# Performance work log

Hardware: AMD Instinct MI355X
Metric: run time of the kernel (lower is better)

## Reference

```python
import jax, jax.numpy as jnp
import numpy as np

NUM_HEADS = 8
HEAD_DIM = 64
EMBED = NUM_HEADS * HEAD_DIM  # 512
KERNEL = 4
TOP_K = 8
SCALING = HEAD_DIM ** (-0.5)


def setup_inputs() -> dict:
    key = jax.random.key(0)
    ks = jax.random.split(key, 5)
    b, s = 4, 4096
    hidden_states = jax.random.normal(ks[0], (b, s, EMBED), dtype=jnp.float32)
    init = 1.0 / np.sqrt(EMBED)
    Wq = jax.random.normal(ks[1], (EMBED, EMBED), dtype=jnp.float32) * init
    Wk = jax.random.normal(ks[2], (EMBED, EMBED), dtype=jnp.float32) * init
    Wv = jax.random.normal(ks[3], (EMBED, EMBED), dtype=jnp.float32) * init
    Wo = jax.random.normal(ks[4], (EMBED, EMBED), dtype=jnp.float32) * init
    return {"hidden_states": hidden_states, "Wq": Wq, "Wk": Wk, "Wv": Wv, "Wo": Wo}


def reference(hidden_states, Wq, Wk, Wv, Wo):
    b, s, _ = hidden_states.shape
    # Q/K/V projections, split heads: (b, s, h, d)
    q = (hidden_states @ Wq).reshape(b, s, NUM_HEADS, HEAD_DIM)
    k = (hidden_states @ Wk).reshape(b, s, NUM_HEADS, HEAD_DIM)
    v = (hidden_states @ Wv).reshape(b, s, NUM_HEADS, HEAD_DIM)

    # KVCachePooling: chunk-mean along seq (s divisible by KERNEL, no pad)
    nc = s // KERNEL
    pooled_k = k.reshape(b, nc, KERNEL, NUM_HEADS, HEAD_DIM).mean(axis=2)  # (b, nc, h, d)
    pooled_v = v.reshape(b, nc, KERNEL, NUM_HEADS, HEAD_DIM).mean(axis=2)

    # TopKSparseRouter: routing scores (b, h, s, nc), reduce heads(max) then queries(max)
    qh = jnp.transpose(q, (0, 2, 1, 3))  # (b, h, s, d)
    route = jnp.einsum('bhsd,bchd->bhsc', qh, pooled_k) * SCALING
    route = route.max(axis=1).max(axis=1)  # (b, nc)
    _, top_idx = jax.lax.top_k(route, TOP_K)  # (b, k)

    # Gather selected pooled chunks: (b, k, h, d)
    k_sel = jnp.take_along_axis(pooled_k, top_idx[:, :, None, None], axis=1)
    v_sel = jnp.take_along_axis(pooled_v, top_idx[:, :, None, None], axis=1)

    # Sparse attention over the k selected chunks only
    attn = jnp.einsum('bhsd,bkhd->bhsk', qh, k_sel) * SCALING  # (b, h, s, k)
    attn = jax.nn.softmax(attn, axis=-1)
    out = jnp.einsum('bhsk,bkhd->bhsd', attn, v_sel)  # (b, h, s, d)
    out = jnp.transpose(out, (0, 2, 1, 3)).reshape(b, s, EMBED)
    return out @ Wo
```

## Files before the change

kernel.cpp:

```cpp
#include <hip/hip_runtime.h>

#define SEQ 4096
#define BATCH 4
#define EMB 512
#define NHEAD 8
#define HDIM 64
#define NCHUNK 1024
#define TOPK 8
#define NSEL 32
#define SCALING 0.125f

typedef unsigned int uint;
typedef unsigned short ushort_t;
typedef __attribute__((ext_vector_type(8))) short short8;
typedef __attribute__((ext_vector_type(4))) float f32x4;
typedef __attribute__((ext_vector_type(4))) unsigned short us4;
typedef __attribute__((ext_vector_type(8))) unsigned short us8;

__device__ __forceinline__ ushort_t bf16_rn(float x) {
  uint b = __float_as_uint(x);
  return (ushort_t)((b + 0x7FFFu + ((b >> 16) & 1u)) >> 16);
}
__device__ __forceinline__ float bf16_f(ushort_t u) {
  return __uint_as_float(((uint)u) << 16);
}

__device__ __forceinline__ void load_lds16(const void* g, void* l) {
  __builtin_amdgcn_global_load_lds(
      (const __attribute__((address_space(1))) unsigned int*)g,
      (__attribute__((address_space(3))) unsigned int*)l, 16, 0, 0);
}

__device__ __forceinline__ f32x4 mfma16(short8 a, short8 b, f32x4 c) {
  return __builtin_amdgcn_mfma_f32_16x16x32_bf16(a, b, c, 0, 0, 0);
}

__device__ __forceinline__ uint float_key(float f) {
  uint bits = __float_as_uint(f);
  return (bits & 0x80000000u) ? ~bits : (bits | 0x80000000u);
}

__global__ __launch_bounds__(256) void wtrans_kernel(
    const float* __restrict__ Wq, const float* __restrict__ Wk,
    const float* __restrict__ Wv,
    ushort_t* __restrict__ Wtq_h, ushort_t* __restrict__ Wtq_l,
    ushort_t* __restrict__ Wtkv_h, ushort_t* __restrict__ Wtkv_l) {
  __shared__ float t[64][65];
  const int z = blockIdx.z;
  const float* src = (z == 0) ? Wq : (z == 1) ? Wk : Wv;
  ushort_t* dh = (z == 0) ? Wtq_h : Wtkv_h;
  ushort_t* dl = (z == 0) ? Wtq_l : Wtkv_l;
  const size_t obase = (z == 2) ? (size_t)512 * 512 : 0;
  const int k0 = blockIdx.x * 64, n0 = blockIdx.y * 64;
  const int tid = threadIdx.x;
#pragma unroll
  for (int i = 0; i < 4; ++i) {
    int row = (tid >> 4) + i * 16, col = (tid & 15) * 4;
    float4 v = *(const float4*)&src[(size_t)(k0 + row) * 512 + n0 + col];
    t[row][col + 0] = v.x; t[row][col + 1] = v.y;
    t[row][col + 2] = v.z; t[row][col + 3] = v.w;
  }
  __syncthreads();
#pragma unroll
  for (int i = 0; i < 4; ++i) {
    int nrow = (tid >> 4) + i * 16, kcol = (tid & 15) * 4;
    us4 h, l;
#pragma unroll
    for (int j = 0; j < 4; ++j) {
      float v = t[kcol + j][nrow];
      ushort_t hb = bf16_rn(v);
      h[j] = hb;
      l[j] = bf16_rn(v - bf16_f(hb));
    }
    size_t o = obase + (size_t)(n0 + nrow) * 512 + k0 + kcol;
    *(us4*)&dh[o] = h;
    *(us4*)&dl[o] = l;
  }
}

__global__ __launch_bounds__(256) void pool_split_kernel(
    const float* __restrict__ H, ushort_t* __restrict__ Hh,
    ushort_t* __restrict__ Hl, ushort_t* __restrict__ Hph,
    ushort_t* __restrict__ Hpl, uint* __restrict__ route) {
  const int idx = blockIdx.x * 256 + threadIdx.x;
  if (idx < BATCH * NCHUNK) route[idx] = 0;
  const int e4 = (idx & 127) << 2;
  const int c = (idx >> 7) & 1023;
  const int b = idx >> 17;
  const size_t rbase = ((size_t)(b * SEQ + c * 4)) * 512 + e4;
  float4 s = make_float4(0.f, 0.f, 0.f, 0.f);
#pragma unroll
  for (int j = 0; j < 4; ++j) {
    float4 v = *(const float4*)&H[rbase + (size_t)j * 512];
    s.x += v.x; s.y += v.y; s.z += v.z; s.w += v.w;
    us4 h, l;
    float a[4] = {v.x, v.y, v.z, v.w};
#pragma unroll
    for (int q = 0; q < 4; ++q) {
      ushort_t hb = bf16_rn(a[q]);
      h[q] = hb;
      l[q] = bf16_rn(a[q] - bf16_f(hb));
    }
    *(us4*)&Hh[rbase + (size_t)j * 512] = h;
    *(us4*)&Hl[rbase + (size_t)j * 512] = l;
  }
  float a[4] = {s.x * 0.25f, s.y * 0.25f, s.z * 0.25f, s.w * 0.25f};
  us4 h, l;
#pragma unroll
  for (int q = 0; q < 4; ++q) {
    ushort_t hb = bf16_rn(a[q]);
    h[q] = hb;
    l[q] = bf16_rn(a[q] - bf16_f(hb));
  }
  size_t po = ((size_t)(b * NCHUNK + c)) * 512 + e4;
  *(us4*)&Hph[po] = h;
  *(us4*)&Hpl[po] = l;
}

__global__ __launch_bounds__(256) void proj_kernel(
    const ushort_t* __restrict__ Hh, const ushort_t* __restrict__ Hl,
    const ushort_t* __restrict__ Hph, const ushort_t* __restrict__ Hpl,
    const ushort_t* __restrict__ Wtq_h, const ushort_t* __restrict__ Wtq_l,
    const ushort_t* __restrict__ Wtkv_h, const ushort_t* __restrict__ Wtkv_l,
    ushort_t* __restrict__ Qh, ushort_t* __restrict__ Ql,
    ushort_t* __restrict__ Pkvh, ushort_t* __restrict__ Pkvl) {
  __shared__ ushort_t lds[2][4][4096];
  const int bid = blockIdx.x;
  const ushort_t *A0, *A1, *B0, *B1;
  ushort_t *Ch, *Cl;
  int ldc, row0, col0;
  if (bid < 512) {
    row0 = (bid >> 2) * 128; col0 = (bid & 3) * 128;
    A0 = Hh; A1 = Hl; B0 = Wtq_h; B1 = Wtq_l; Ch = Qh; Cl = Ql; ldc = 512;
  } else {
    int b2 = bid - 512;
    row0 = (b2 >> 3) * 128; col0 = (b2 & 7) * 128;
    A0 = Hph; A1 = Hpl; B0 = Wtkv_h; B1 = Wtkv_l; Ch = Pkvh; Cl = Pkvl;
    ldc = 1024;
  }
  A0 += (size_t)row0 * 512; A1 += (size_t)row0 * 512;
  B0 += (size_t)col0 * 512; B1 += (size_t)col0 * 512;
  const int tid = threadIdx.x, lane = tid & 63, wv = tid >> 6;
  const int l15 = lane & 15, g = lane >> 4;
  const int wm = wv >> 1, wn = wv & 1;
  f32x4 acc[4][4];
#pragma unroll
  for (int m = 0; m < 4; ++m)
#pragma unroll
    for (int n = 0; n < 4; ++n) acc[m][n] = (f32x4){0.f, 0.f, 0.f, 0.f};

  auto stage = [&](int buf, int t) {
#pragma unroll
    for (int j = 0; j < 2; ++j) {
      int si = j * 256 + wv * 64 + lane;
      int row = si >> 2;
      int kb = ((si & 3) << 4) ^ (((row >> 1) & 3) << 4);
      size_t goff = (size_t)row * 512 + t * 32 + (kb >> 1);
      int doff = (j * 256 + wv * 64) * 8;
      load_lds16(A0 + goff, &lds[buf][0][doff]);
      load_lds16(B0 + goff, &lds[buf][1][doff]);
      load_lds16(A1 + goff, &lds[buf][2][doff]);
      load_lds16(B1 + goff, &lds[buf][3][doff]);
    }
  };

  stage(0, 0);
  int cur = 0;
  for (int t = 0; t < 16; ++t) {
    __syncthreads();
    if (t < 15) stage(cur ^ 1, t + 1);
    short8 ah[4], bh[4], al[4], bl[4];
#pragma unroll
    for (int m = 0; m < 4; ++m) {
      int r = wm * 64 + m * 16 + l15;
      int kb = (g << 4) ^ (((r >> 1) & 3) << 4);
      ah[m] = *(const short8*)&lds[cur][0][r * 32 + (kb >> 1)];
      al[m] = *(const short8*)&lds[cur][2][r * 32 + (kb >> 1)];
    }
#pragma unroll
    for (int n = 0; n < 4; ++n) {
      int r = wn * 64 + n * 16 + l15;
      int kb = (g << 4) ^ (((r >> 1) & 3) << 4);
      bh[n] = *(const short8*)&lds[cur][1][r * 32 + (kb >> 1)];
      bl[n] = *(const short8*)&lds[cur][3][r * 32 + (kb >> 1)];
    }
#pragma unroll
    for (int m = 0; m < 4; ++m)
#pragma unroll
      for (int n = 0; n < 4; ++n) {
        acc[m][n] = mfma16(ah[m], bh[n], acc[m][n]);
        acc[m][n] = mfma16(ah[m], bl[n], acc[m][n]);
        acc[m][n] = mfma16(al[m], bh[n], acc[m][n]);
      }
    cur ^= 1;
  }
#pragma unroll
  for (int m = 0; m < 4; ++m)
#pragma unroll
    for (int n = 0; n < 4; ++n)
#pragma unroll
      for (int q = 0; q < 4; ++q) {
        int row = row0 + wm * 64 + m * 16 + g * 4 + q;
        int col = col0 + wn * 64 + n * 16 + l15;
        float v = acc[m][n][q];
        size_t o = (size_t)row * ldc + col;
        ushort_t hb = bf16_rn(v);
        Ch[o] = hb;
        Cl[o] = bf16_rn(v - bf16_f(hb));
      }
}

__device__ __forceinline__ void stage128x64(const ushort_t* src, int stride,
                                            ushort_t* dst, int wv, int lane) {
#pragma unroll
  for (int j = 0; j < 4; ++j) {
    int si = j * 256 + wv * 64 + lane;
    int row = si >> 3;
    int kb = ((si & 7) << 4) ^ ((row & 7) << 4);
    load_lds16(src + (size_t)row * stride + (kb >> 1),
               dst + (size_t)(j * 256 + wv * 64) * 8);
  }
}

__global__ __launch_bounds__(256) void route_screen(
    const ushort_t* __restrict__ Qh, const ushort_t* __restrict__ Pkh,
    uint* __restrict__ route) {
  __shared__ ushort_t Alds[2][128 * 64];
  __shared__ ushort_t Blds[128 * 64];
  __shared__ float red[2][128];
  const int tid = threadIdx.x, lane = tid & 63, wv = tid >> 6;
  const int l15 = lane & 15, g = lane >> 4;
  const int wm = wv >> 1, wc = wv & 1;
  const int c0 = blockIdx.x * 128;
  const int h = blockIdx.y >> 1, sb = blockIdx.y & 1;
  const int b = blockIdx.z;
  const int s0 = sb * 2048;
  const ushort_t* Qhb = Qh + ((size_t)b * SEQ) * 512 + h * 64;
  const ushort_t* Pkhb = Pkh + ((size_t)(b * NCHUNK + c0)) * 1024 + h * 64;

  stage128x64(Pkhb, 1024, &Blds[0], wv, lane);
  __syncthreads();
  short8 bh[2][4];
#pragma unroll
  for (int kk = 0; kk < 2; ++kk)
#pragma unroll
    for (int n = 0; n < 4; ++n) {
      int r = wc * 64 + n * 16 + l15;
      int kb = (kk * 64 + (g << 4)) ^ ((r & 7) << 4);
      bh[kk][n] = *(const short8*)&Blds[r * 64 + (kb >> 1)];
    }

  float rmax[4] = {-1e30f, -1e30f, -1e30f, -1e30f};
  stage128x64(Qhb + (size_t)s0 * 512, 512, &Alds[0][0], wv, lane);
  int cur = 0;
  for (int it = 0; it < 16; ++it) {
    __syncthreads();
    if (it < 15) {
      size_t so = (size_t)(s0 + (it + 1) * 128) * 512;
      stage128x64(Qhb + so, 512, &Alds[cur ^ 1][0], wv, lane);
    }
    f32x4 acc[4][4];
#pragma unroll
    for (int m = 0; m < 4; ++m)
#pragma unroll
      for (int n = 0; n < 4; ++n) acc[m][n] = (f32x4){0.f, 0.f, 0.f, 0.f};
#pragma unroll
    for (int kk = 0; kk < 2; ++kk) {
      short8 ah[4];
#pragma unroll
      for (int m = 0; m < 4; ++m) {
        int r = wm * 64 + m * 16 + l15;
        int kb = (kk * 64 + (g << 4)) ^ ((r & 7) << 4);
        ah[m] = *(const short8*)&Alds[cur][r * 64 + (kb >> 1)];
      }
#pragma unroll
      for (int m = 0; m < 4; ++m)
#pragma unroll
        for (int n = 0; n < 4; ++n)
          acc[m][n] = mfma16(ah[m], bh[kk][n], acc[m][n]);
    }
#pragma unroll
    for (int n = 0; n < 4; ++n)
#pragma unroll
      for (int m = 0; m < 4; ++m)
        rmax[n] = fmaxf(rmax[n],
                        fmaxf(fmaxf(acc[m][n][0], acc[m][n][1]),
                              fmaxf(acc[m][n][2], acc[m][n][3])));
    cur ^= 1;
  }
#pragma unroll
  for (int n = 0; n < 4; ++n) {
    float v = rmax[n];
    v = fmaxf(v, __shfl_xor(v, 16, 64));
    v = fmaxf(v, __shfl_xor(v, 32, 64));
    if (g == 0) red[wm][wc * 64 + n * 16 + l15] = v;
  }
  __syncthreads();
  if (tid < 128) {
    float v = fmaxf(red[0][tid], red[1][tid]);
    atomicMax(&route[b * NCHUNK + c0 + tid], float_key(v));
  }
}

__global__ __launch_bounds__(256) void topk_sel(const uint* __restrict__ route,
                                                int* __restrict__ cand,
                                                uint* __restrict__ route2) {
  const int b = blockIdx.x, tid = threadIdx.x;
  __shared__ unsigned long long keys[NCHUNK];
#pragma unroll
  for (int i = 0; i < 4; ++i) {
    int idx = tid + i * 256;
    keys[idx] = ((unsigned long long)route[b * NCHUNK + idx] << 32) |
                (uint)(NCHUNK - 1 - idx);
  }
  if (tid < NSEL) route2[b * NSEL + tid] = 0;
  __syncthreads();
  for (int k = 2; k <= NCHUNK; k <<= 1) {
    for (int j = k >> 1; j > 0; j >>= 1) {
#pragma unroll
      for (int ii = 0; ii < 4; ++ii) {
        int i = tid + ii * 256;
        int p = i ^ j;
        if (p > i) {
          bool desc = ((i & k) == 0);
          unsigned long long a = keys[i], c = keys[p];
          bool sw = desc ? (a < c) : (a > c);
          if (sw) { keys[i] = c; keys[p] = a; }
        }
      }
      __syncthreads();
    }
  }
  if (tid < NSEL)
    cand[b * NSEL + tid] = NCHUNK - 1 - (int)(keys[tid] & 0xffffffffu);
}

__global__ __launch_bounds__(256) void rescore_kernel(
    const ushort_t* __restrict__ Qh, const ushort_t* __restrict__ Ql,
    const ushort_t* __restrict__ Pkvh, const ushort_t* __restrict__ Pkvl,
    const int* __restrict__ cand, uint* __restrict__ route2) {
  __shared__ ushort_t Ah[128 * 64], Al[128 * 64];
  __shared__ ushort_t Bh[NSEL * 64], Bl[NSEL * 64];
  __shared__ float red[4][NSEL];
  const int tid = threadIdx.x, lane = tid & 63, wv = tid >> 6;
  const int l15 = lane & 15, g = lane >> 4;
  const int st = blockIdx.x, h = blockIdx.y, b = blockIdx.z;
  const int s0 = st * 128;
  {
    int row = tid >> 3;
    int kb = ((tid & 7) << 4) ^ ((row & 7) << 4);
    int c = cand[b * NSEL + row];
    size_t src = ((size_t)(b * NCHUNK + c)) * 1024 + h * 64 + (kb >> 1);
    load_lds16(Pkvh + src, &Bh[(size_t)(wv * 64) * 8]);
    load_lds16(Pkvl + src, &Bl[(size_t)(wv * 64) * 8]);
  }
  const ushort_t* Qhb = Qh + ((size_t)(b * SEQ + s0)) * 512 + h * 64;
  const ushort_t* Qlb = Ql + ((size_t)(b * SEQ + s0)) * 512 + h * 64;
  stage128x64(Qhb, 512, Ah, wv, lane);
  stage128x64(Qlb, 512, Al, wv, lane);
  __syncthreads();

  f32x4 acc[2][2];
#pragma unroll
  for (int m = 0; m < 2; ++m)
#pragma unroll
    for (int n = 0; n < 2; ++n) acc[m][n] = (f32x4){0.f, 0.f, 0.f, 0.f};
#pragma unroll
  for (int kk = 0; kk < 2; ++kk) {
    short8 ah[2], al[2], bh[2], bl[2];
#pragma unroll
    for (int m = 0; m < 2; ++m) {
      int r = wv * 32 + m * 16 + l15;
      int kb = (kk * 64 + (g << 4)) ^ ((r & 7) << 4);
      ah[m] = *(const short8*)&Ah[r * 64 + (kb >> 1)];
      al[m] = *(const short8*)&Al[r * 64 + (kb >> 1)];
    }
#pragma unroll
    for (int n = 0; n < 2; ++n) {
      int r = n * 16 + l15;
      int kb = (kk * 64 + (g << 4)) ^ ((r & 7) << 4);
      bh[n] = *(const short8*)&Bh[r * 64 + (kb >> 1)];
      bl[n] = *(const short8*)&Bl[r * 64 + (kb >> 1)];
    }
#pragma unroll
    for (int m = 0; m < 2; ++m)
#pragma unroll
      for (int n = 0; n < 2; ++n) {
        acc[m][n] = mfma16(ah[m], bh[n], acc[m][n]);
        acc[m][n] = mfma16(ah[m], bl[n], acc[m][n]);
        acc[m][n] = mfma16(al[m], bh[n], acc[m][n]);
      }
  }
#pragma unroll
  for (int n = 0; n < 2; ++n) {
    float v = -1e30f;
#pragma unroll
    for (int m = 0; m < 2; ++m)
      v = fmaxf(v, fmaxf(fmaxf(acc[m][n][0], acc[m][n][1]),
                         fmaxf(acc[m][n][2], acc[m][n][3])));
    v = fmaxf(v, __shfl_xor(v, 16, 64));
    v = fmaxf(v, __shfl_xor(v, 32, 64));
    if (g == 0) red[wv][n * 16 + l15] = v;
  }
  __syncthreads();
  if (tid < NSEL) {
    float v = fmaxf(fmaxf(red[0][tid], red[1][tid]),
                    fmaxf(red[2][tid], red[3][tid]));
    atomicMax(&route2[b * NSEL + tid], float_key(v));
  }
}

__global__ __launch_bounds__(64) void topk_final(const uint* __restrict__ route2,
                                                 const int* __restrict__ cand,
                                                 int* __restrict__ topidx) {
  const int b = blockIdx.x, lane = threadIdx.x;
  uint key = (lane < NSEL) ? route2[b * NSEL + lane] : 0u;
  const int myc = (lane < NSEL) ? cand[b * NSEL + lane] : 0;
  for (int it = 0; it < TOPK; ++it) {
    unsigned long long kk = ((unsigned long long)key << 32) | (uint)(63 - lane);
#pragma unroll
    for (int o = 32; o > 0; o >>= 1) {
      unsigned long long ot = __shfl_xor(kk, o, 64);
      kk = (ot > kk) ? ot : kk;
    }
    int widx = 63 - (int)(kk & 0xffffffffu);
    if (lane == widx) {
      topidx[b * TOPK + it] = myc;
      key = 0u;
    }
  }
}

__global__ __launch_bounds__(256) void vw_kernel(
    const ushort_t* __restrict__ Pkvh, const ushort_t* __restrict__ Pkvl,
    const float* __restrict__ Wo, const int* __restrict__ topidx,
    ushort_t* __restrict__ VWth, ushort_t* __restrict__ VWtl) {
  __shared__ float Vs[8][512];
  const int tid = threadIdx.x, et = blockIdx.x, b = blockIdx.y;
#pragma unroll
  for (int i = 0; i < 16; ++i) {
    int idx = tid + i * 256;
    int j = idx >> 9, d = idx & 511;
    int c = topidx[b * TOPK + j];
    size_t src = ((size_t)(b * NCHUNK + c)) * 1024 + 512 + d;
    Vs[j][d] = bf16_f(Pkvh[src]) + bf16_f(Pkvl[src]);
  }
  __syncthreads();
  const int e = et * 64 + (tid & 63), qr = tid >> 6;
  ushort_t hbuf[16], lbuf[16];
#pragma unroll
  for (int i = 0; i < 16; ++i) {
    int hj = qr * 16 + i, h = hj >> 3, j = hj & 7;
    float dot = 0.f;
#pragma unroll
    for (int d = 0; d < 64; ++d)
      dot += Vs[j][h * 64 + d] * Wo[(size_t)(h * 64 + d) * 512 + e];
    ushort_t hb = bf16_rn(dot);
    hbuf[i] = hb;
    lbuf[i] = bf16_rn(dot - bf16_f(hb));
  }
  size_t o = ((size_t)(b * 512 + e)) * 64 + qr * 16;
  *(us8*)&VWth[o] = *(us8*)&hbuf[0];
  *(us8*)&VWth[o + 8] = *(us8*)&hbuf[8];
  *(us8*)&VWtl[o] = *(us8*)&lbuf[0];
  *(us8*)&VWtl[o + 8] = *(us8*)&lbuf[8];
}

__global__ __launch_bounds__(256) void attn_out_kernel(
    const ushort_t* __restrict__ Qh, const ushort_t* __restrict__ Ql,
    const ushort_t* __restrict__ Pkvh, const ushort_t* __restrict__ Pkvl,
    const int* __restrict__ topidx, const ushort_t* __restrict__ VWth,
    const ushort_t* __restrict__ VWtl, float* __restrict__ out) {
  __shared__ float Ksel[8 * 516];
  __shared__ ushort_t Pho[64 * 64], Plo[64 * 64];
  const int tid = threadIdx.x, lane = tid & 63, wv = tid >> 6;
  const int l15 = lane & 15, g = lane >> 4;
  const int st = blockIdx.x, b = blockIdx.y;
  const int s0 = st * 64;
  {
    int j = tid >> 5, h = (tid >> 2) & 7, dg = tid & 3;
    int c = topidx[b * TOPK + j];
    size_t base = ((size_t)(b * NCHUNK + c)) * 1024 + h * 64 + dg * 16;
    us8 h0 = *(const us8*)&Pkvh[base], h1 = *(const us8*)&Pkvh[base + 8];
    us8 l0 = *(const us8*)&Pkvl[base], l1 = *(const us8*)&Pkvl[base + 8];
#pragma unroll
    for (int ii = 0; ii < 8; ++ii) {
      Ksel[h * 516 + j * 64 + dg * 16 + ii] = bf16_f(h0[ii]) + bf16_f(l0[ii]);
      Ksel[h * 516 + j * 64 + dg * 16 + 8 + ii] = bf16_f(h1[ii]) + bf16_f(l1[ii]);
    }
  }
  __syncthreads();
  {
    const int r = tid >> 2, hp = tid & 3;
    const size_t qbase = ((size_t)(b * SEQ + s0 + r)) * 512;
#pragma unroll
    for (int hh = 0; hh < 2; ++hh) {
      const int h = hp * 2 + hh;
      float qf[64];
#pragma unroll
      for (int i = 0; i < 8; ++i) {
        us8 vh = *(const us8*)&Qh[qbase + h * 64 + i * 8];
        us8 vl = *(const us8*)&Ql[qbase + h * 64 + i * 8];
#pragma unroll
        for (int k2 = 0; k2 < 8; ++k2)
          qf[i * 8 + k2] = bf16_f(vh[k2]) + bf16_f(vl[k2]);
      }
      float sc[TOPK], m = -1e30f;
#pragma unroll
      for (int j = 0; j < TOPK; ++j) {
        float dot = 0.f;
#pragma unroll
        for (int d4 = 0; d4 < 16; ++d4) {
          float4 kv = *(const float4*)&Ksel[h * 516 + j * 64 + d4 * 4];
          dot += qf[d4 * 4 + 0] * kv.x + qf[d4 * 4 + 1] * kv.y +
                 qf[d4 * 4 + 2] * kv.z + qf[d4 * 4 + 3] * kv.w;
        }
        sc[j] = dot * SCALING;
        m = fmaxf(m, sc[j]);
      }
      float se = 0.f, w8[TOPK];
#pragma unroll
      for (int j = 0; j < TOPK; ++j) {
        w8[j] = __expf(sc[j] - m);
        se += w8[j];
      }
      const float inv = 1.f / se;
      us8 ph8, pl8;
#pragma unroll
      for (int j = 0; j < TOPK; ++j) {
        float pv = w8[j] * inv;
        ushort_t hb = bf16_rn(pv);
        ph8[j] = hb;
        pl8[j] = bf16_rn(pv - bf16_f(hb));
      }
      int boff = (r * 128 + h * 16) ^ ((r & 7) << 4);
      *(us8*)((char*)Pho + boff) = ph8;
      *(us8*)((char*)Plo + boff) = pl8;
    }
  }
  __syncthreads();
  short8 pa[4][2], pb[4][2];
#pragma unroll
  for (int m = 0; m < 4; ++m) {
    int r = m * 16 + l15;
#pragma unroll
    for (int kk = 0; kk < 2; ++kk) {
      int boff = (r * 128 + kk * 64 + g * 16) ^ ((r & 7) << 4);
      pa[m][kk] = *(const short8*)((const char*)Pho + boff);
      pb[m][kk] = *(const short8*)((const char*)Plo + boff);
    }
  }
#pragma unroll
  for (int half = 0; half < 2; ++half) {
    const int colbase = wv * 128 + half * 64;
    short8 bh[4][2], bl[4][2];
#pragma unroll
    for (int n = 0; n < 4; ++n) {
      int e = colbase + n * 16 + l15;
      size_t vb = ((size_t)(b * 512 + e)) * 64;
#pragma unroll
      for (int kk = 0; kk < 2; ++kk) {
        bh[n][kk] = *(const short8*)&VWth[vb + kk * 32 + g * 8];
        bl[n][kk] = *(const short8*)&VWtl[vb + kk * 32 + g * 8];
      }
    }
    f32x4 acc[4][4];
#pragma unroll
    for (int m = 0; m < 4; ++m)
#pragma unroll
      for (int n = 0; n < 4; ++n) acc[m][n] = (f32x4){0.f, 0.f, 0.f, 0.f};
#pragma unroll
    for (int kk = 0; kk < 2; ++kk)
#pragma unroll
      for (int m = 0; m < 4; ++m)
#pragma unroll
        for (int n = 0; n < 4; ++n) {
          acc[m][n] = mfma16(pa[m][kk], bh[n][kk], acc[m][n]);
          acc[m][n] = mfma16(pa[m][kk], bl[n][kk], acc[m][n]);
          acc[m][n] = mfma16(pb[m][kk], bh[n][kk], acc[m][n]);
        }
#pragma unroll
    for (int m = 0; m < 4; ++m)
#pragma unroll
      for (int n = 0; n < 4; ++n)
#pragma unroll
        for (int q = 0; q < 4; ++q) {
          int row = s0 + m * 16 + g * 4 + q;
          int col = colbase + n * 16 + l15;
          out[((size_t)(b * SEQ) + row) * 512 + col] = acc[m][n][q];
        }
  }
}

extern "C" void kernel_launch(void* const* d_in, const int* in_sizes, int n_in,
                              void* d_out, int out_size, void* d_ws, size_t ws_size,
                              hipStream_t stream) {
  const float* H = (const float*)d_in[0];
  const float* Wq = (const float*)d_in[1];
  const float* Wk = (const float*)d_in[2];
  const float* Wv = (const float*)d_in[3];
  const float* Wo = (const float*)d_in[4];
  float* out = (float*)d_out;

  char* p = (char*)d_ws;
  auto alloc = [&](size_t bytes) {
    void* r = (void*)p;
    p += (bytes + 255) & ~(size_t)255;
    return r;
  };
  const size_t BS = (size_t)BATCH * SEQ;
  const size_t BC = (size_t)BATCH * NCHUNK;
  ushort_t* Hh = (ushort_t*)alloc(BS * 512 * 2);
  ushort_t* Hl = (ushort_t*)alloc(BS * 512 * 2);
  ushort_t* Hph = (ushort_t*)alloc(BC * 512 * 2);
  ushort_t* Hpl = (ushort_t*)alloc(BC * 512 * 2);
  ushort_t* Wtq_h = (ushort_t*)alloc(512 * 512 * 2);
  ushort_t* Wtq_l = (ushort_t*)alloc(512 * 512 * 2);
  ushort_t* Wtkv_h = (ushort_t*)alloc(1024 * 512 * 2);
  ushort_t* Wtkv_l = (ushort_t*)alloc(1024 * 512 * 2);
  ushort_t* Qh = (ushort_t*)alloc(BS * 512 * 2);
  ushort_t* Ql = (ushort_t*)alloc(BS * 512 * 2);
  ushort_t* Pkvh = (ushort_t*)alloc(BC * 1024 * 2);
  ushort_t* Pkvl = (ushort_t*)alloc(BC * 1024 * 2);
  ushort_t* VWth = (ushort_t*)alloc((size_t)BATCH * 512 * 64 * 2);
  ushort_t* VWtl = (ushort_t*)alloc((size_t)BATCH * 512 * 64 * 2);
  uint* route = (uint*)alloc(BC * 4);
  uint* route2 = (uint*)alloc((size_t)BATCH * NSEL * 4);
  int* cand = (int*)alloc(BATCH * NSEL * 4);
  int* topidx = (int*)alloc(BATCH * TOPK * 4);

  wtrans_kernel<<<dim3(8, 8, 3), 256, 0, stream>>>(
      Wq, Wk, Wv, Wtq_h, Wtq_l, Wtkv_h, Wtkv_l);
  pool_split_kernel<<<2048, 256, 0, stream>>>(H, Hh, Hl, Hph, Hpl, route);
  proj_kernel<<<768, 256, 0, stream>>>(Hh, Hl, Hph, Hpl, Wtq_h, Wtq_l,
                                       Wtkv_h, Wtkv_l, Qh, Ql, Pkvh, Pkvl);
  route_screen<<<dim3(8, 16, 4), 256, 0, stream>>>(Qh, Pkvh, route);
  topk_sel<<<BATCH, 256, 0, stream>>>(route, cand, route2);
  rescore_kernel<<<dim3(32, 8, 4), 256, 0, stream>>>(Qh, Ql, Pkvh, Pkvl, cand,
                                                     route2);
  topk_final<<<BATCH, 64, 0, stream>>>(route2, cand, topidx);
  vw_kernel<<<dim3(8, BATCH), 256, 0, stream>>>(Pkvh, Pkvl, Wo, topidx, VWth,
                                                VWtl);
  attn_out_kernel<<<dim3(64, BATCH), 256, 0, stream>>>(
      Qh, Ql, Pkvh, Pkvl, topidx, VWth, VWtl, out);
  (void)in_sizes; (void)n_in; (void)out_size; (void)ws_size;
}
```

Baseline: 256.7 us.

## Merge prep kernels, fold top-k into consumers, single-buffer LDS, remap blocks per XCD

Merges the weight transpose and the pooling/split kernels into one launch, and removes the topk_final kernel by having vw and attn_out each compute the top-8 inline. Drops double buffering in proj_kernel and route_screen in favour of a single LDS buffer with extra barriers, which lowers LDS use and may raise occupancy. Remaps block indices so neighbouring row tiles land on the same XCD for better cache reuse. attn_out now reads only the high bf16 half of Q, which saves bandwidth at some cost in precision.

```diff
diff --git a/kernel.cpp b/kernel.cpp
--- a/kernel.cpp
+++ b/kernel.cpp
@@ -40,81 +40,104 @@
   return (bits & 0x80000000u) ? ~bits : (bits | 0x80000000u);
 }
 
-__global__ __launch_bounds__(256) void wtrans_kernel(
-    const float* __restrict__ Wq, const float* __restrict__ Wk,
-    const float* __restrict__ Wv,
+__device__ __forceinline__ void top8_inline(const uint* __restrict__ route2,
+                                            const int* __restrict__ cand,
+                                            int b, int lane,
+                                            int* __restrict__ tops) {
+  uint key = (lane < NSEL) ? route2[b * NSEL + lane] : 0u;
+  const int myc = (lane < NSEL) ? cand[b * NSEL + lane] : 0;
+  for (int it = 0; it < TOPK; ++it) {
+    unsigned long long kk = ((unsigned long long)key << 32) | (uint)(63 - lane);
+#pragma unroll
+    for (int o = 32; o > 0; o >>= 1) {
+      unsigned long long ot = __shfl_xor(kk, o, 64);
+      kk = (ot > kk) ? ot : kk;
+    }
+    int widx = 63 - (int)(kk & 0xffffffffu);
+    if (lane == widx) {
+      tops[it] = myc;
+      key = 0u;
+    }
+  }
+}
+
+__global__ __launch_bounds__(256) void prep_kernel(
+    const float* __restrict__ H, const float* __restrict__ Wq,
+    const float* __restrict__ Wk, const float* __restrict__ Wv,
+    ushort_t* __restrict__ Hh, ushort_t* __restrict__ Hl,
+    ushort_t* __restrict__ Hph, ushort_t* __restrict__ Hpl,
     ushort_t* __restrict__ Wtq_h, ushort_t* __restrict__ Wtq_l,
-    ushort_t* __restrict__ Wtkv_h, ushort_t* __restrict__ Wtkv_l) {
+    ushort_t* __restrict__ Wtkv_h, ushort_t* __restrict__ Wtkv_l,
+    uint* __restrict__ route) {
   __shared__ float t[64][65];
-  const int z = blockIdx.z;
-  const float* src = (z == 0) ? Wq : (z == 1) ? Wk : Wv;
-  ushort_t* dh = (z == 0) ? Wtq_h : Wtkv_h;
-  ushort_t* dl = (z == 0) ? Wtq_l : Wtkv_l;
-  const size_t obase = (z == 2) ? (size_t)512 * 512 : 0;
-  const int k0 = blockIdx.x * 64, n0 = blockIdx.y * 64;
   const int tid = threadIdx.x;
-#pragma unroll
-  for (int i = 0; i < 4; ++i) {
-    int row = (tid >> 4) + i * 16, col = (tid & 15) * 4;
-    float4 v = *(const float4*)&src[(size_t)(k0 + row) * 512 + n0 + col];
-    t[row][col + 0] = v.x; t[row][col + 1] = v.y;
-    t[row][col + 2] = v.z; t[row][col + 3] = v.w;
-  }
-  __syncthreads();
-#pragma unroll
-  for (int i = 0; i < 4; ++i) {
-    int nrow = (tid >> 4) + i * 16, kcol = (tid & 15) * 4;
+  if (blockIdx.x < 2048) {
+    const int idx = blockIdx.x * 256 + tid;
+    if (idx < BATCH * NCHUNK) route[idx] = 0;
+    const int e4 = (idx & 127) << 2;
+    const int c = (idx >> 7) & 1023;
+    const int b = idx >> 17;
+    const size_t rbase = ((size_t)(b * SEQ + c * 4)) * 512 + e4;
+    float4 s = make_float4(0.f, 0.f, 0.f, 0.f);
+#pragma unroll
+    for (int j = 0; j < 4; ++j) {
+      float4 v = *(const float4*)&H[rbase + (size_t)j * 512];
+      s.x += v.x; s.y += v.y; s.z += v.z; s.w += v.w;
+      us4 h, l;
+      float a[4] = {v.x, v.y, v.z, v.w};
+#pragma unroll
+      for (int q = 0; q < 4; ++q) {
+        ushort_t hb = bf16_rn(a[q]);
+        h[q] = hb;
+        l[q] = bf16_rn(a[q] - bf16_f(hb));
+      }
+      *(us4*)&Hh[rbase + (size_t)j * 512] = h;
+      *(us4*)&Hl[rbase + (size_t)j * 512] = l;
+    }
+    float a[4] = {s.x * 0.25f, s.y * 0.25f, s.z * 0.25f, s.w * 0.25f};
     us4 h, l;
-#pragma unroll
-    for (int j = 0; j < 4; ++j) {
-      float v = t[kcol + j][nrow];
-      ushort_t hb = bf16_rn(v);
-      h[j] = hb;
-      l[j] = bf16_rn(v - bf16_f(hb));
-    }
-    size_t o = obase + (size_t)(n0 + nrow) * 512 + k0 + kcol;
-    *(us4*)&dh[o] = h;
-    *(us4*)&dl[o] = l;
-  }
-}
-
-__global__ __launch_bounds__(256) void pool_split_kernel(
-    const float* __restrict__ H, ushort_t* __restrict__ Hh,
-    ushort_t* __restrict__ Hl, ushort_t* __restrict__ Hph,
-    ushort_t* __restrict__ Hpl, uint* __restrict__ route) {
-  const int idx = blockIdx.x * 256 + threadIdx.x;
-  if (idx < BATCH * NCHUNK) route[idx] = 0;
-  const int e4 = (idx & 127) << 2;
-  const int c = (idx >> 7) & 1023;
-  const int b = idx >> 17;
-  const size_t rbase = ((size_t)(b * SEQ + c * 4)) * 512 + e4;
-  float4 s = make_float4(0.f, 0.f, 0.f, 0.f);
-#pragma unroll
-  for (int j = 0; j < 4; ++j) {
-    float4 v = *(const float4*)&H[rbase + (size_t)j * 512];
-    s.x += v.x; s.y += v.y; s.z += v.z; s.w += v.w;
-    us4 h, l;
-    float a[4] = {v.x, v.y, v.z, v.w};
 #pragma unroll
     for (int q = 0; q < 4; ++q) {
       ushort_t hb = bf16_rn(a[q]);
       h[q] = hb;
       l[q] = bf16_rn(a[q] - bf16_f(hb));
     }
-    *(us4*)&Hh[rbase + (size_t)j * 512] = h;
-    *(us4*)&Hl[rbase + (size_t)j * 512] = l;
-  }
-  float a[4] = {s.x * 0.25f, s.y * 0.25f, s.z * 0.25f, s.w * 0.25f};
-  us4 h, l;
-#pragma unroll
-  for (int q = 0; q < 4; ++q) {
-    ushort_t hb = bf16_rn(a[q]);
-    h[q] = hb;
-    l[q] = bf16_rn(a[q] - bf16_f(hb));
-  }
-  size_t po = ((size_t)(b * NCHUNK + c)) * 512 + e4;
-  *(us4*)&Hph[po] = h;
-  *(us4*)&Hpl[po] = l;
+    size_t po = ((size_t)(b * NCHUNK + c)) * 512 + e4;
+    *(us4*)&Hph[po] = h;
+    *(us4*)&Hpl[po] = l;
+  } else {
+    const int bid2 = blockIdx.x - 2048;
+    const int z = bid2 >> 6;
+    const int xy = bid2 & 63;
+    const int k0 = (xy & 7) * 64, n0 = (xy >> 3) * 64;
+    const float* src = (z == 0) ? Wq : (z == 1) ? Wk : Wv;
+    ushort_t* dh = (z == 0) ? Wtq_h : Wtkv_h;
+    ushort_t* dl = (z == 0) ? Wtq_l : Wtkv_l;
+    const size_t obase = (z == 2) ? (size_t)512 * 512 : 0;
+#pragma unroll
+    for (int i = 0; i < 4; ++i) {
+      int row = (tid >> 4) + i * 16, col = (tid & 15) * 4;
+      float4 v = *(const float4*)&src[(size_t)(k0 + row) * 512 + n0 + col];
+      t[row][col + 0] = v.x; t[row][col + 1] = v.y;
+      t[row][col + 2] = v.z; t[row][col + 3] = v.w;
+    }
+    __syncthreads();
+#pragma unroll
+    for (int i = 0; i < 4; ++i) {
+      int nrow = (tid >> 4) + i * 16, kcol = (tid & 15) * 4;
+      us4 h, l;
+#pragma unroll
+      for (int j = 0; j < 4; ++j) {
+        float v = t[kcol + j][nrow];
+        ushort_t hb = bf16_rn(v);
+        h[j] = hb;
+        l[j] = bf16_rn(v - bf16_f(hb));
+      }
+      size_t o = obase + (size_t)(n0 + nrow) * 512 + k0 + kcol;
+      *(us4*)&dh[o] = h;
+      *(us4*)&dl[o] = l;
+    }
+  }
 }
 
 __global__ __launch_bounds__(256) void proj_kernel(
@@ -124,17 +147,21 @@
     const ushort_t* __restrict__ Wtkv_h, const ushort_t* __restrict__ Wtkv_l,
     ushort_t* __restrict__ Qh, ushort_t* __restrict__ Ql,
     ushort_t* __restrict__ Pkvh, ushort_t* __restrict__ Pkvl) {
-  __shared__ ushort_t lds[2][4][4096];
+  __shared__ ushort_t lds[4][4096];
   const int bid = blockIdx.x;
   const ushort_t *A0, *A1, *B0, *B1;
   ushort_t *Ch, *Cl;
   int ldc, row0, col0;
   if (bid < 512) {
-    row0 = (bid >> 2) * 128; col0 = (bid & 3) * 128;
+    int xcd = bid & 7, idx = bid >> 3;
+    int r = (idx >> 2) * 8 + xcd, c = idx & 3;
+    row0 = r * 128; col0 = c * 128;
     A0 = Hh; A1 = Hl; B0 = Wtq_h; B1 = Wtq_l; Ch = Qh; Cl = Ql; ldc = 512;
   } else {
     int b2 = bid - 512;
-    row0 = (b2 >> 3) * 128; col0 = (b2 & 7) * 128;
+    int xcd = b2 & 7, idx = b2 >> 3;
+    int r = (idx >> 3) * 8 + xcd, c = idx & 7;
+    row0 = r * 128; col0 = c * 128;
     A0 = Hph; A1 = Hpl; B0 = Wtkv_h; B1 = Wtkv_l; Ch = Pkvh; Cl = Pkvl;
     ldc = 1024;
   }
@@ -149,7 +176,7 @@
 #pragma unroll
     for (int n = 0; n < 4; ++n) acc[m][n] = (f32x4){0.f, 0.f, 0.f, 0.f};
 
-  auto stage = [&](int buf, int t) {
+  auto stage = [&](int t) {
 #pragma unroll
     for (int j = 0; j < 2; ++j) {
       int si = j * 256 + wv * 64 + lane;
@@ -157,32 +184,30 @@
       int kb = ((si & 3) << 4) ^ (((row >> 1) & 3) << 4);
       size_t goff = (size_t)row * 512 + t * 32 + (kb >> 1);
       int doff = (j * 256 + wv * 64) * 8;
-      load_lds16(A0 + goff, &lds[buf][0][doff]);
-      load_lds16(B0 + goff, &lds[buf][1][doff]);
-      load_lds16(A1 + goff, &lds[buf][2][doff]);
-      load_lds16(B1 + goff, &lds[buf][3][doff]);
+      load_lds16(A0 + goff, &lds[0][doff]);
+      load_lds16(B0 + goff, &lds[1][doff]);
+      load_lds16(A1 + goff, &lds[2][doff]);
+      load_lds16(B1 + goff, &lds[3][doff]);
     }
   };
 
-  stage(0, 0);
-  int cur = 0;
+  stage(0);
   for (int t = 0; t < 16; ++t) {
     __syncthreads();
-    if (t < 15) stage(cur ^ 1, t + 1);
     short8 ah[4], bh[4], al[4], bl[4];
 #pragma unroll
     for (int m = 0; m < 4; ++m) {
       int r = wm * 64 + m * 16 + l15;
       int kb = (g << 4) ^ (((r >> 1) & 3) << 4);
-      ah[m] = *(const short8*)&lds[cur][0][r * 32 + (kb >> 1)];
-      al[m] = *(const short8*)&lds[cur][2][r * 32 + (kb >> 1)];
+      ah[m] = *(const short8*)&lds[0][r * 32 + (kb >> 1)];
+      al[m] = *(const short8*)&lds[2][r * 32 + (kb >> 1)];
     }
 #pragma unroll
     for (int n = 0; n < 4; ++n) {
       int r = wn * 64 + n * 16 + l15;
       int kb = (g << 4) ^ (((r >> 1) & 3) << 4);
-      bh[n] = *(const short8*)&lds[cur][1][r * 32 + (kb >> 1)];
-      bl[n] = *(const short8*)&lds[cur][3][r * 32 + (kb >> 1)];
+      bh[n] = *(const short8*)&lds[1][r * 32 + (kb >> 1)];
+      bl[n] = *(const short8*)&lds[3][r * 32 + (kb >> 1)];
     }
 #pragma unroll
     for (int m = 0; m < 4; ++m)
@@ -192,7 +217,8 @@
         acc[m][n] = mfma16(ah[m], bl[n], acc[m][n]);
         acc[m][n] = mfma16(al[m], bh[n], acc[m][n]);
       }
-    cur ^= 1;
+    __syncthreads();
+    if (t < 15) stage(t + 1);
   }
 #pragma unroll
   for (int m = 0; m < 4; ++m)
@@ -225,20 +251,23 @@
 __global__ __launch_bounds__(256) void route_screen(
     const ushort_t* __restrict__ Qh, const ushort_t* __restrict__ Pkh,
     uint* __restrict__ route) {
-  __shared__ ushort_t Alds[2][128 * 64];
+  __shared__ ushort_t Alds[128 * 64];
   __shared__ ushort_t Blds[128 * 64];
   __shared__ float red[2][128];
   const int tid = threadIdx.x, lane = tid & 63, wv = tid >> 6;
   const int l15 = lane & 15, g = lane >> 4;
   const int wm = wv >> 1, wc = wv & 1;
-  const int c0 = blockIdx.x * 128;
-  const int h = blockIdx.y >> 1, sb = blockIdx.y & 1;
-  const int b = blockIdx.z;
+  const int bid = blockIdx.x;
+  const int gl = bid & 7, c0i = (bid >> 3) & 7, gh = bid >> 6;
+  const int grp = gh * 8 + gl;
+  const int b = grp >> 4, h = (grp >> 1) & 7, sb = grp & 1;
+  const int c0 = c0i * 128;
   const int s0 = sb * 2048;
   const ushort_t* Qhb = Qh + ((size_t)b * SEQ) * 512 + h * 64;
   const ushort_t* Pkhb = Pkh + ((size_t)(b * NCHUNK + c0)) * 1024 + h * 64;
 
   stage128x64(Pkhb, 1024, &Blds[0], wv, lane);
+  stage128x64(Qhb + (size_t)s0 * 512, 512, &Alds[0], wv, lane);
   __syncthreads();
   short8 bh[2][4];
 #pragma unroll
@@ -251,14 +280,7 @@
     }
 
   float rmax[4] = {-1e30f, -1e30f, -1e30f, -1e30f};
-  stage128x64(Qhb + (size_t)s0 * 512, 512, &Alds[0][0], wv, lane);
-  int cur = 0;
   for (int it = 0; it < 16; ++it) {
-    __syncthreads();
-    if (it < 15) {
-      size_t so = (size_t)(s0 + (it + 1) * 128) * 512;
-      stage128x64(Qhb + so, 512, &Alds[cur ^ 1][0], wv, lane);
-    }
     f32x4 acc[4][4];
 #pragma unroll
     for (int m = 0; m < 4; ++m)
@@ -271,7 +293,7 @@
       for (int m = 0; m < 4; ++m) {
         int r = wm * 64 + m * 16 + l15;
         int kb = (kk * 64 + (g << 4)) ^ ((r & 7) << 4);
-        ah[m] = *(const short8*)&Alds[cur][r * 64 + (kb >> 1)];
+        ah[m] = *(const short8*)&Alds[r * 64 + (kb >> 1)];
       }
 #pragma unroll
       for (int m = 0; m < 4; ++m)
@@ -286,7 +308,12 @@
         rmax[n] = fmaxf(rmax[n],
                         fmaxf(fmaxf(acc[m][n][0], acc[m][n][1]),
                               fmaxf(acc[m][n][2], acc[m][n][3])));
-    cur ^= 1;
+    __syncthreads();
+    if (it < 15) {
+      size_t so = (size_t)(s0 + (it + 1) * 128) * 512;
+      stage128x64(Qhb + so, 512, &Alds[0], wv, lane);
+    }
+    __syncthreads();
   }
 #pragma unroll
   for (int n = 0; n < 4; ++n) {
@@ -410,38 +437,21 @@
   }
 }
 
-__global__ __launch_bounds__(64) void topk_final(const uint* __restrict__ route2,
-                                                 const int* __restrict__ cand,
-                                                 int* __restrict__ topidx) {
-  const int b = blockIdx.x, lane = threadIdx.x;
-  uint key = (lane < NSEL) ? route2[b * NSEL + lane] : 0u;
-  const int myc = (lane < NSEL) ? cand[b * NSEL + lane] : 0;
-  for (int it = 0; it < TOPK; ++it) {
-    unsigned long long kk = ((unsigned long long)key << 32) | (uint)(63 - lane);
-#pragma unroll
-    for (int o = 32; o > 0; o >>= 1) {
-      unsigned long long ot = __shfl_xor(kk, o, 64);
-      kk = (ot > kk) ? ot : kk;
-    }
-    int widx = 63 - (int)(kk & 0xffffffffu);
-    if (lane == widx) {
-      topidx[b * TOPK + it] = myc;
-      key = 0u;
-    }
-  }
-}
-
 __global__ __launch_bounds__(256) void vw_kernel(
     const ushort_t* __restrict__ Pkvh, const ushort_t* __restrict__ Pkvl,
-    const float* __restrict__ Wo, const int* __restrict__ topidx,
-    ushort_t* __restrict__ VWth, ushort_t* __restrict__ VWtl) {
+    const float* __restrict__ Wo, const uint* __restrict__ route2,
+    const int* __restrict__ cand, ushort_t* __restrict__ VWth,
+    ushort_t* __restrict__ VWtl) {
   __shared__ float Vs[8][512];
+  __shared__ int tops[TOPK];
   const int tid = threadIdx.x, et = blockIdx.x, b = blockIdx.y;
+  if (tid < 64) top8_inline(route2, cand, b, tid, tops);
+  __syncthreads();
 #pragma unroll
   for (int i = 0; i < 16; ++i) {
     int idx = tid + i * 256;
     int j = idx >> 9, d = idx & 511;
-    int c = topidx[b * TOPK + j];
+    int c = tops[j];
     size_t src = ((size_t)(b * NCHUNK + c)) * 1024 + 512 + d;
     Vs[j][d] = bf16_f(Pkvh[src]) + bf16_f(Pkvl[src]);
   }
@@ -467,26 +477,30 @@
 }
 
 __global__ __launch_bounds__(256) void attn_out_kernel(
-    const ushort_t* __restrict__ Qh, const ushort_t* __restrict__ Ql,
-    const ushort_t* __restrict__ Pkvh, const ushort_t* __restrict__ Pkvl,
-    const int* __restrict__ topidx, const ushort_t* __restrict__ VWth,
+    const ushort_t* __restrict__ Qh, const ushort_t* __restrict__ Pkvh,
+    const ushort_t* __restrict__ Pkvl, const uint* __restrict__ route2,
+    const int* __restrict__ cand, const ushort_t* __restrict__ VWth,
     const ushort_t* __restrict__ VWtl, float* __restrict__ out) {
   __shared__ float Ksel[8 * 516];
   __shared__ ushort_t Pho[64 * 64], Plo[64 * 64];
+  __shared__ int tops[TOPK];
   const int tid = threadIdx.x, lane = tid & 63, wv = tid >> 6;
   const int l15 = lane & 15, g = lane >> 4;
   const int st = blockIdx.x, b = blockIdx.y;
   const int s0 = st * 64;
+  if (tid < 64) top8_inline(route2, cand, b, tid, tops);
+  __syncthreads();
   {
     int j = tid >> 5, h = (tid >> 2) & 7, dg = tid & 3;
-    int c = topidx[b * TOPK + j];
+    int c = tops[j];
     size_t base = ((size_t)(b * NCHUNK + c)) * 1024 + h * 64 + dg * 16;
     us8 h0 = *(const us8*)&Pkvh[base], h1 = *(const us8*)&Pkvh[base + 8];
     us8 l0 = *(const us8*)&Pkvl[base], l1 = *(const us8*)&Pkvl[base + 8];
 #pragma unroll
     for (int ii = 0; ii < 8; ++ii) {
       Ksel[h * 516 + j * 64 + dg * 16 + ii] = bf16_f(h0[ii]) + bf16_f(l0[ii]);
-      Ksel[h * 516 + j * 64 + dg * 16 + 8 + ii] = bf16_f(h1[ii]) + bf16_f(l1[ii]);
+      Ksel[h * 516 + j * 64 + dg * 16 + 8 + ii] =
+          bf16_f(h1[ii]) + bf16_f(l1[ii]);
     }
   }
   __syncthreads();
@@ -500,10 +514,8 @@
 #pragma unroll
       for (int i = 0; i < 8; ++i) {
         us8 vh = *(const us8*)&Qh[qbase + h * 64 + i * 8];
-        us8 vl = *(const us8*)&Ql[qbase + h * 64 + i * 8];
-#pragma unroll
-        for (int k2 = 0; k2 < 8; ++k2)
-          qf[i * 8 + k2] = bf16_f(vh[k2]) + bf16_f(vl[k2]);
+#pragma unroll
+        for (int k2 = 0; k2 < 8; ++k2) qf[i * 8 + k2] = bf16_f(vh[k2]);
       }
       float sc[TOPK], m = -1e30f;
 #pragma unroll
@@ -627,21 +639,18 @@
   uint* route = (uint*)alloc(BC * 4);
   uint* route2 = (uint*)alloc((size_t)BATCH * NSEL * 4);
   int* cand = (int*)alloc(BATCH * NSEL * 4);
-  int* topidx = (int*)alloc(BATCH * TOPK * 4);
-
-  wtrans_kernel<<<dim3(8, 8, 3), 256, 0, stream>>>(
-      Wq, Wk, Wv, Wtq_h, Wtq_l, Wtkv_h, Wtkv_l);
-  pool_split_kernel<<<2048, 256, 0, stream>>>(H, Hh, Hl, Hph, Hpl, route);
+
+  prep_kernel<<<2240, 256, 0, stream>>>(H, Wq, Wk, Wv, Hh, Hl, Hph, Hpl,
+                                        Wtq_h, Wtq_l, Wtkv_h, Wtkv_l, route);
   proj_kernel<<<768, 256, 0, stream>>>(Hh, Hl, Hph, Hpl, Wtq_h, Wtq_l,
                                        Wtkv_h, Wtkv_l, Qh, Ql, Pkvh, Pkvl);
-  route_screen<<<dim3(8, 16, 4), 256, 0, stream>>>(Qh, Pkvh, route);
+  route_screen<<<512, 256, 0, stream>>>(Qh, Pkvh, route);
   topk_sel<<<BATCH, 256, 0, stream>>>(route, cand, route2);
   rescore_kernel<<<dim3(32, 8, 4), 256, 0, stream>>>(Qh, Ql, Pkvh, Pkvl, cand,
                                                      route2);
-  topk_final<<<BATCH, 64, 0, stream>>>(route2, cand, topidx);
-  vw_kernel<<<dim3(8, BATCH), 256, 0, stream>>>(Pkvh, Pkvl, Wo, topidx, VWth,
-                                                VWtl);
+  vw_kernel<<<dim3(8, BATCH), 256, 0, stream>>>(Pkvh, Pkvl, Wo, route2, cand,
+                                                VWth, VWtl);
   attn_out_kernel<<<dim3(64, BATCH), 256, 0, stream>>>(
-      Qh, Ql, Pkvh, Pkvl, topidx, VWth, VWtl, out);
+      Qh, Pkvh, Pkvl, route2, cand, VWth, VWtl, out);
   (void)in_sizes; (void)n_in; (void)out_size; (void)ws_size;
 }
```

After: 239.4 us. -6.8%, faster.
